# Optimization experiments

Measured on AMD Instinct MI355X. Metric: run time of the kernel, lower is better.

Reference implementation:

```python
import jax, jax.numpy as jnp
import numpy as np

VOCAB, BLOCK, D, H, E, TOPK = 50257, 2048, 1024, 8, 8, 2
HD = D // H  # head_size = 128


def _layernorm(x, g, b, eps=1e-5):
    mu = jnp.mean(x, axis=-1, keepdims=True)
    var = jnp.mean(jnp.square(x - mu), axis=-1, keepdims=True)
    return (x - mu) * jax.lax.rsqrt(var + eps) * g + b


def setup_inputs() -> dict:
    key = jax.random.key(0)
    ks = jax.random.split(key, 12)
    s = 0.02
    return {
        "idx": jax.random.randint(ks[0], (4, BLOCK), 0, VOCAB),
        "tok_table": jax.random.normal(ks[1], (VOCAB, D), jnp.float32) * s,
        "pos_table": jax.random.normal(ks[2], (BLOCK, D), jnp.float32) * s,
        "Wq": jax.random.normal(ks[3], (H, D, HD), jnp.float32) * s,
        "Wk": jax.random.normal(ks[4], (H, D, HD), jnp.float32) * s,
        "Wv": jax.random.normal(ks[5], (H, D, HD), jnp.float32) * s,
        "Wo": jax.random.normal(ks[6], (D, D), jnp.float32) * s,
        "bo": jnp.zeros((D,), jnp.float32),
        "g1": jnp.ones((D,), jnp.float32),
        "b1": jnp.zeros((D,), jnp.float32),
        "g2": jnp.ones((D,), jnp.float32),
        "b2": jnp.zeros((D,), jnp.float32),
        "Wr": jax.random.normal(ks[7], (D, E), jnp.float32) * s,
        "br": jnp.zeros((E,), jnp.float32),
        "Wn": jax.random.normal(ks[8], (D, E), jnp.float32) * s,
        "bn": jnp.zeros((E,), jnp.float32),
    }


def reference(idx, tok_table, pos_table, Wq, Wk, Wv, Wo, bo, g1, b1, g2, b2, Wr, br, Wn, bn):
    B, T = idx.shape
    x = tok_table[idx] + pos_table[:T]  # [B,T,D]

    # --- multi-head causal self-attention (dropout off / eval mode) ---
    xn = _layernorm(x, g1, b1)
    q = jnp.einsum('btc,hcd->bhtd', xn, Wq)
    k = jnp.einsum('btc,hcd->bhtd', xn, Wk)
    v = jnp.einsum('btc,hcd->bhtd', xn, Wv)
    # NOTE: original scales by C**-0.5 where C = n_embed (not head_size)
    wei = jnp.einsum('bhtd,bhsd->bhts', q, k) * (D ** -0.5)
    causal = jnp.tril(jnp.ones((T, T), bool))
    wei = jnp.where(causal, wei, -jnp.inf)
    wei = jax.nn.softmax(wei, axis=-1)
    attn = jnp.einsum('bhts,bhsd->bhtd', wei, v)  # [B,H,T,HD]
    attn = attn.transpose(0, 2, 1, 3).reshape(B, T, D)  # concat heads
    x = x + attn @ Wo + bo  # residual

    x_norm = _layernorm(x, g2, b2)

    # --- noisy top-k router ---
    logits = x_norm @ Wr + br          # [B,T,E]
    noise_logits = x_norm @ Wn + bn    # [B,T,E]
    noise = jax.random.normal(jax.random.key(42), logits.shape, logits.dtype)
    noisy = logits + noise * jax.nn.softplus(noise_logits)
    top_vals, indices = jax.lax.top_k(noisy, TOPK)  # [B,T,K]
    probs_k = jax.nn.softmax(top_vals, axis=-1)     # softmax over -inf-scattered logits == softmax over top-k
    router_probs = jnp.sum(jax.nn.one_hot(indices, E, dtype=probs_k.dtype) * probs_k[..., None], axis=-2)

    return (x_norm, router_probs, indices, x)
```

## Files before the change

### kernel.cpp

```cpp
#include <hip/hip_runtime.h>
#include <math.h>
#include <stdint.h>

typedef __attribute__((ext_vector_type(8))) _Float16 f16x8;
typedef __attribute__((ext_vector_type(4))) _Float16 f16x4;
typedef __attribute__((ext_vector_type(4))) float f32x4;

__device__ __forceinline__ void split_f16(float x, _Float16& h, _Float16& l) {
  h = (_Float16)x;
  l = (_Float16)((x - (float)h) * 2048.0f);
}

__device__ __forceinline__ void gld16(const void* g, void* l) {
  __builtin_amdgcn_global_load_lds(
      (const __attribute__((address_space(1))) void*)g,
      (__attribute__((address_space(3))) void*)l, 16, 0, 0);
}

__device__ __forceinline__ void threefry2x32_42(uint32_t x0, uint32_t x1,
                                                uint32_t& o0, uint32_t& o1) {
  const uint32_t k0 = 0u, k1 = 42u;
  const uint32_t k2 = k0 ^ k1 ^ 0x1BD11BDAu;
  x0 += k0; x1 += k1;
#define TF_R(r) { x0 += x1; x1 = (x1 << (r)) | (x1 >> (32 - (r))); x1 ^= x0; }
  TF_R(13) TF_R(15) TF_R(26) TF_R(6)
  x0 += k1; x1 += k2 + 1u;
  TF_R(17) TF_R(29) TF_R(16) TF_R(24)
  x0 += k2; x1 += k0 + 2u;
  TF_R(13) TF_R(15) TF_R(26) TF_R(6)
  x0 += k0; x1 += k1 + 3u;
  TF_R(17) TF_R(29) TF_R(16) TF_R(24)
  x0 += k1; x1 += k2 + 4u;
  TF_R(13) TF_R(15) TF_R(26) TF_R(6)
  x0 += k2; x1 += k0 + 5u;
#undef TF_R
  o0 = x0; o1 = x1;
}

__device__ __forceinline__ float jax_erfinv_f32(float x) {
  float xx = __fmul_rn(x, x);
  float w = -log1pf(-xx);
  float p;
  if (w < 5.0f) {
    w = __fadd_rn(w, -2.5f);
    p = 2.81022636e-08f;
    p = __fadd_rn(3.43273939e-07f, __fmul_rn(p, w));
    p = __fadd_rn(-3.5233877e-06f, __fmul_rn(p, w));
    p = __fadd_rn(-4.39150654e-06f, __fmul_rn(p, w));
    p = __fadd_rn(0.00021858087f, __fmul_rn(p, w));
    p = __fadd_rn(-0.00125372503f, __fmul_rn(p, w));
    p = __fadd_rn(-0.00417768164f, __fmul_rn(p, w));
    p = __fadd_rn(0.246640727f, __fmul_rn(p, w));
    p = __fadd_rn(1.50140941f, __fmul_rn(p, w));
  } else {
    w = __fadd_rn(sqrtf(w), -3.0f);
    p = -0.000200214257f;
    p = __fadd_rn(0.000100950558f, __fmul_rn(p, w));
    p = __fadd_rn(0.00134934322f, __fmul_rn(p, w));
    p = __fadd_rn(-0.00367342844f, __fmul_rn(p, w));
    p = __fadd_rn(0.00573950773f, __fmul_rn(p, w));
    p = __fadd_rn(-0.0076224613f, __fmul_rn(p, w));
    p = __fadd_rn(0.00943887047f, __fmul_rn(p, w));
    p = __fadd_rn(1.00167406f, __fmul_rn(p, w));
    p = __fadd_rn(2.83297682f, __fmul_rn(p, w));
  }
  return __fmul_rn(p, x);
}

__device__ __forceinline__ float jax_noise(uint32_t n) {
  uint32_t o0, o1;
  threefry2x32_42(0u, n, o0, o1);
  uint32_t bits = o0 ^ o1;
  uint32_t fb = (bits >> 9) | 0x3F800000u;
  float f = __fadd_rn(__uint_as_float(fb), -1.0f);
  const float lo = __uint_as_float(0xBF7FFFFFu);
  float u = __fadd_rn(__fmul_rn(f, 2.0f), lo);
  u = fmaxf(lo, u);
  return __fmul_rn(__uint_as_float(0x3FB504F3u), jax_erfinv_f32(u));
}

__device__ __forceinline__ float block_sum_256(float v, float* buf) {
  #pragma unroll
  for (int off = 32; off > 0; off >>= 1) v += __shfl_down(v, off, 64);
  int lane = threadIdx.x & 63;
  int w = threadIdx.x >> 6;
  if (lane == 0) buf[w] = v;
  __syncthreads();
  return buf[0] + buf[1] + buf[2] + buf[3];
}

__global__ __launch_bounds__(128) void k_wsplit(
    const float* __restrict__ Wq, const float* __restrict__ Wk,
    const float* __restrict__ Wv, const float* __restrict__ Wo,
    _Float16* __restrict__ wqt_h, _Float16* __restrict__ wqt_l,
    _Float16* __restrict__ wot_h, _Float16* __restrict__ wot_l) {
  int z = blockIdx.x, tid = threadIdx.x;
  const float* src;
  int ldn, n;
  _Float16 *dh, *dl;
  if (z < 24) {
    int which = z >> 3, h = z & 7;
    src = ((which == 0) ? Wq : (which == 1) ? Wk : Wv) + (size_t)h * 1024 * 128;
    ldn = 128; n = tid;
    dh = wqt_h + (size_t)z * 128 * 1024 + (size_t)n * 1024;
    dl = wqt_l + (size_t)z * 128 * 1024 + (size_t)n * 1024;
  } else {
    int zz = z - 24;
    src = Wo; ldn = 1024; n = zz * 128 + tid;
    dh = wot_h + (size_t)n * 1024;
    dl = wot_l + (size_t)n * 1024;
  }
  for (int k0 = 0; k0 < 1024; k0 += 16) {
    f16x8 hv0, hv1, lv0, lv1;
    #pragma unroll
    for (int j = 0; j < 8; ++j) {
      _Float16 hh, ll;
      split_f16(src[(size_t)(k0 + j) * ldn + n], hh, ll);
      hv0[j] = hh; lv0[j] = ll;
    }
    #pragma unroll
    for (int j = 0; j < 8; ++j) {
      _Float16 hh, ll;
      split_f16(src[(size_t)(k0 + 8 + j) * ldn + n], hh, ll);
      hv1[j] = hh; lv1[j] = ll;
    }
    *(f16x8*)(dh + k0) = hv0; *(f16x8*)(dh + k0 + 8) = hv1;
    *(f16x8*)(dl + k0) = lv0; *(f16x8*)(dl + k0 + 8) = lv1;
  }
}

__global__ __launch_bounds__(256) void k_embed_ln1(
    const int* __restrict__ idx, const float* __restrict__ tok,
    const float* __restrict__ pos, const float* __restrict__ g1,
    const float* __restrict__ b1, float* __restrict__ x_out,
    _Float16* __restrict__ xnh, _Float16* __restrict__ xnl) {
  __shared__ float bufA[4], bufB[4];
  int r = blockIdx.x;
  int t = r & 2047;
  int token = idx[r];
  int c4 = threadIdx.x;
  float4 tv = *((const float4*)(tok + (size_t)token * 1024) + c4);
  float4 pv = *((const float4*)(pos + (size_t)t * 1024) + c4);
  float4 xv = make_float4(tv.x + pv.x, tv.y + pv.y, tv.z + pv.z, tv.w + pv.w);
  *((float4*)(x_out + (size_t)r * 1024) + c4) = xv;
  float mu = block_sum_256(xv.x + xv.y + xv.z + xv.w, bufA) * (1.0f / 1024.0f);
  float d0 = xv.x - mu, d1 = xv.y - mu, d2 = xv.z - mu, d3 = xv.w - mu;
  float var = block_sum_256(d0*d0 + d1*d1 + d2*d2 + d3*d3, bufB) * (1.0f / 1024.0f);
  float rs = rsqrtf(var + 1e-5f);
  float4 gv = *((const float4*)g1 + c4);
  float4 bv = *((const float4*)b1 + c4);
  float xn0 = d0*rs*gv.x + bv.x, xn1 = d1*rs*gv.y + bv.y;
  float xn2 = d2*rs*gv.z + bv.z, xn3 = d3*rs*gv.w + bv.w;
  f16x4 hv, lv;
  _Float16 hh, ll;
  split_f16(xn0, hh, ll); hv[0] = hh; lv[0] = ll;
  split_f16(xn1, hh, ll); hv[1] = hh; lv[1] = ll;
  split_f16(xn2, hh, ll); hv[2] = hh; lv[2] = ll;
  split_f16(xn3, hh, ll); hv[3] = hh; lv[3] = ll;
  *(f16x4*)(xnh + (size_t)r * 1024 + c4 * 4) = hv;
  *(f16x4*)(xnl + (size_t)r * 1024 + c4 * 4) = lv;
}

__global__ __launch_bounds__(256) void k_ln2(
    const float* __restrict__ x, const float* __restrict__ g2,
    const float* __restrict__ b2, float* __restrict__ xn_out) {
  __shared__ float bufA[4], bufB[4];
  int r = blockIdx.x;
  int c4 = threadIdx.x;
  float4 xv = *((const float4*)(x + (size_t)r * 1024) + c4);
  float mu = block_sum_256(xv.x + xv.y + xv.z + xv.w, bufA) * (1.0f / 1024.0f);
  float d0 = xv.x - mu, d1 = xv.y - mu, d2 = xv.z - mu, d3 = xv.w - mu;
  float var = block_sum_256(d0*d0 + d1*d1 + d2*d2 + d3*d3, bufB) * (1.0f / 1024.0f);
  float rs = rsqrtf(var + 1e-5f);
  float4 gv = *((const float4*)g2 + c4);
  float4 bv = *((const float4*)b2 + c4);
  float4 xn = make_float4(d0*rs*gv.x + bv.x, d1*rs*gv.y + bv.y,
                          d2*rs*gv.z + bv.z, d3*rs*gv.w + bv.w);
  *((float4*)(xn_out + (size_t)r * 1024) + c4) = xn;
}

__global__ __launch_bounds__(256) void k_qkv(
    const _Float16* __restrict__ xnh, const _Float16* __restrict__ xnl,
    const _Float16* __restrict__ wth, const _Float16* __restrict__ wtl,
    _Float16* __restrict__ qh, _Float16* __restrict__ ql,
    _Float16* __restrict__ kh, _Float16* __restrict__ kl,
    _Float16* __restrict__ vth, _Float16* __restrict__ vtl) {
  __shared__ __align__(16) _Float16 Ah[128 * 32], Al[128 * 32];
  __shared__ __align__(16) _Float16 Bh[128 * 32], Bl[128 * 32];
  int z = blockIdx.x;
  int which = z >> 3, h = z & 7;
  int m0 = blockIdx.y * 128;
  int tid = threadIdx.x, w = tid >> 6, lane = tid & 63;
  const _Float16* bsh = wth + (size_t)z * 128 * 1024;
  const _Float16* bsl = wtl + (size_t)z * 128 * 1024;
  f32x4 om[2][8], oc[2][8];
  const f32x4 zero4 = {0.f, 0.f, 0.f, 0.f};
  #pragma unroll
  for (int mr = 0; mr < 2; ++mr)
    #pragma unroll
    for (int nb = 0; nb < 8; ++nb) { om[mr][nb] = zero4; oc[mr][nb] = zero4; }

  for (int k0 = 0; k0 < 1024; k0 += 32) {
    __syncthreads();
    #pragma unroll
    for (int i2 = 0; i2 < 2; ++i2) {
      int r = w * 32 + i2 * 16 + (lane >> 2);
      int gs = (lane & 3) ^ ((r >> 1) & 3);
      size_t ao = (size_t)(m0 + r) * 1024 + k0 + gs * 8;
      size_t bo_ = (size_t)r * 1024 + k0 + gs * 8;
      gld16(xnh + ao, &Ah[(w * 32 + i2 * 16) * 32]);
      gld16(xnl + ao, &Al[(w * 32 + i2 * 16) * 32]);
      gld16(bsh + bo_, &Bh[(w * 32 + i2 * 16) * 32]);
      gld16(bsl + bo_, &Bl[(w * 32 + i2 * 16) * 32]);
    }
    asm volatile("s_waitcnt vmcnt(0)" ::: "memory");
    __syncthreads();
    f16x8 ah[2], al[2];
    #pragma unroll
    for (int mr = 0; mr < 2; ++mr) {
      int arow = w * 32 + mr * 16 + (lane & 15);
      int ag = (lane >> 4) ^ ((arow >> 1) & 3);
      ah[mr] = *(f16x8*)&Ah[arow * 32 + ag * 8];
      al[mr] = *(f16x8*)&Al[arow * 32 + ag * 8];
    }
    #pragma unroll
    for (int nb = 0; nb < 8; ++nb) {
      int brow = nb * 16 + (lane & 15);
      int bg = (lane >> 4) ^ ((brow >> 1) & 3);
      f16x8 b8h = *(f16x8*)&Bh[brow * 32 + bg * 8];
      f16x8 b8l = *(f16x8*)&Bl[brow * 32 + bg * 8];
      #pragma unroll
      for (int mr = 0; mr < 2; ++mr) {
        om[mr][nb] = __builtin_amdgcn_mfma_f32_16x16x32_f16(ah[mr], b8h, om[mr][nb], 0, 0, 0);
        oc[mr][nb] = __builtin_amdgcn_mfma_f32_16x16x32_f16(ah[mr], b8l, oc[mr][nb], 0, 0, 0);
        oc[mr][nb] = __builtin_amdgcn_mfma_f32_16x16x32_f16(al[mr], b8h, oc[mr][nb], 0, 0, 0);
      }
    }
  }
  int bb = m0 >> 11, tb = m0 & 2047;
  if (which < 2) {
    _Float16* OH = (which == 0) ? qh : kh;
    _Float16* OL = (which == 0) ? ql : kl;
    size_t base = (size_t)(bb * 8 + h) * 2048 * 128;
    #pragma unroll
    for (int mr = 0; mr < 2; ++mr)
      #pragma unroll
      for (int r2 = 0; r2 < 4; ++r2) {
        int t = tb + w * 32 + mr * 16 + ((lane >> 4) << 2) + r2;
        size_t roff = base + (size_t)t * 128 + (lane & 15);
        #pragma unroll
        for (int nb = 0; nb < 8; ++nb) {
          float v = om[mr][nb][r2] + oc[mr][nb][r2] * (1.0f / 2048.0f);
          _Float16 hh, ll;
          split_f16(v, hh, ll);
          OH[roff + nb * 16] = hh;
          OL[roff + nb * 16] = ll;
        }
      }
  } else {
    size_t base = (size_t)(bb * 8 + h) * 128 * 2048;
    #pragma unroll
    for (int mr = 0; mr < 2; ++mr) {
      int t4 = tb + w * 32 + mr * 16 + ((lane >> 4) << 2);
      #pragma unroll
      for (int nb = 0; nb < 8; ++nb) {
        int col = nb * 16 + (lane & 15);
        size_t off = base + (size_t)col * 2048 + t4;
        f16x4 hv, lv;
        #pragma unroll
        for (int r2 = 0; r2 < 4; ++r2) {
          _Float16 hh, ll;
          split_f16(om[mr][nb][r2] + oc[mr][nb][r2] * (1.0f / 2048.0f), hh, ll);
          hv[r2] = hh; lv[r2] = ll;
        }
        *(f16x4*)(vth + off) = hv;
        *(f16x4*)(vtl + off) = lv;
      }
    }
  }
}

__global__ __launch_bounds__(256) void k_proj_res(
    const _Float16* __restrict__ ah_, const _Float16* __restrict__ al_,
    const _Float16* __restrict__ wth, const _Float16* __restrict__ wtl,
    const float* __restrict__ bo, float* __restrict__ x_io) {
  __shared__ __align__(16) _Float16 Ah[128 * 64], Al[128 * 64];
  __shared__ __align__(16) _Float16 Bh[128 * 64], Bl[128 * 64];
  int n0 = blockIdx.x * 128;
  int m0 = blockIdx.y * 128;
  int tid = threadIdx.x, w = tid >> 6, lane = tid & 63;
  f32x4 om[2][8], oc[2][8];
  const f32x4 zero4 = {0.f, 0.f, 0.f, 0.f};
  #pragma unroll
  for (int mr = 0; mr < 2; ++mr)
    #pragma unroll
    for (int nb = 0; nb < 8; ++nb) { om[mr][nb] = zero4; oc[mr][nb] = zero4; }

  for (int k0 = 0; k0 < 1024; k0 += 64) {
    __syncthreads();
    #pragma unroll
    for (int i2 = 0; i2 < 4; ++i2) {
      int r = w * 32 + i2 * 8 + (lane >> 3);
      int gs = (lane & 7) ^ (r & 7);
      size_t ao = (size_t)(m0 + r) * 1024 + k0 + gs * 8;
      size_t bo_ = (size_t)(n0 + r) * 1024 + k0 + gs * 8;
      gld16(ah_ + ao, &Ah[(w * 32 + i2 * 8) * 64]);
      gld16(al_ + ao, &Al[(w * 32 + i2 * 8) * 64]);
      gld16(wth + bo_, &Bh[(w * 32 + i2 * 8) * 64]);
      gld16(wtl + bo_, &Bl[(w * 32 + i2 * 8) * 64]);
    }
    asm volatile("s_waitcnt vmcnt(0)" ::: "memory");
    __syncthreads();
    #pragma unroll
    for (int k2 = 0; k2 < 2; ++k2) {
      f16x8 ah[2], al[2];
      #pragma unroll
      for (int mr = 0; mr < 2; ++mr) {
        int arow = w * 32 + mr * 16 + (lane & 15);
        int ag = (k2 * 4 + (lane >> 4)) ^ (arow & 7);
        ah[mr] = *(f16x8*)&Ah[arow * 64 + ag * 8];
        al[mr] = *(f16x8*)&Al[arow * 64 + ag * 8];
      }
      #pragma unroll
      for (int nb = 0; nb < 8; ++nb) {
        int brow = nb * 16 + (lane & 15);
        int bg = (k2 * 4 + (lane >> 4)) ^ (brow & 7);
        f16x8 b8h = *(f16x8*)&Bh[brow * 64 + bg * 8];
        f16x8 b8l = *(f16x8*)&Bl[brow * 64 + bg * 8];
        #pragma unroll
        for (int mr = 0; mr < 2; ++mr) {
          om[mr][nb] = __builtin_amdgcn_mfma_f32_16x16x32_f16(ah[mr], b8h, om[mr][nb], 0, 0, 0);
          oc[mr][nb] = __builtin_amdgcn_mfma_f32_16x16x32_f16(ah[mr], b8l, oc[mr][nb], 0, 0, 0);
          oc[mr][nb] = __builtin_amdgcn_mfma_f32_16x16x32_f16(al[mr], b8h, oc[mr][nb], 0, 0, 0);
        }
      }
    }
  }
  #pragma unroll
  for (int mr = 0; mr < 2; ++mr)
    #pragma unroll
    for (int nb = 0; nb < 8; ++nb) {
      int col = n0 + nb * 16 + (lane & 15);
      float bov = bo[col];
      #pragma unroll
      for (int r2 = 0; r2 < 4; ++r2) {
        int gm = m0 + w * 32 + mr * 16 + ((lane >> 4) << 2) + r2;
        float* p = x_io + (size_t)gm * 1024 + col;
        *p += om[mr][nb][r2] + oc[mr][nb][r2] * (1.0f / 2048.0f) + bov;
      }
    }
}

__global__ __launch_bounds__(256) void k_attn(
    const _Float16* __restrict__ qhp, const _Float16* __restrict__ qlp,
    const _Float16* __restrict__ khp, const _Float16* __restrict__ klp,
    const _Float16* __restrict__ vthp, const _Float16* __restrict__ vtlp,
    _Float16* __restrict__ attn_h, _Float16* __restrict__ attn_l) {
  __shared__ __align__(16) _Float16 Ksh[2][32 * 128];
  __shared__ __align__(16) _Float16 Ksl[2][32 * 128];
  __shared__ __align__(16) _Float16 Vh[2][128 * 32];
  __shared__ __align__(16) _Float16 Vl[2][128 * 32];
  __shared__ __align__(16) _Float16 Ph4[4][16 * 32];
  __shared__ __align__(16) _Float16 Pl4[4][16 * 32];

  int h = blockIdx.y, b = blockIdx.z;
  int qs = blockIdx.x;
  int tid = threadIdx.x;
  int w = tid >> 6, lane = tid & 63;

  size_t bh = (size_t)(b * 8 + h) * 2048 * 128;
  const _Float16* qhb = qhp + bh;
  const _Float16* qlb = qlp + bh;
  const _Float16* khb = khp + bh;
  const _Float16* klb = klp + bh;
  const _Float16* vhb = vthp + bh;
  const _Float16* vlb = vtlp + bh;
  _Float16* Ph = &Ph4[w][0];
  _Float16* Pl = &Pl4[w][0];

  const f32x4 zero4 = {0.f, 0.f, 0.f, 0.f};

  auto stage = [&](int cur, int j0) {
    #pragma unroll
    for (int i2 = 0; i2 < 2; ++i2) {
      int r = w * 8 + i2 * 4 + (lane >> 4);
      int gs = (lane & 15) ^ (r & 7);
      size_t go = (size_t)(j0 + r) * 128 + gs * 8;
      gld16(khb + go, &Ksh[cur][(w * 8 + i2 * 4) * 128]);
      gld16(klb + go, &Ksl[cur][(w * 8 + i2 * 4) * 128]);
    }
    #pragma unroll
    for (int i2 = 0; i2 < 2; ++i2) {
      int r = w * 32 + i2 * 16 + (lane >> 2);
      int gs = (lane & 3) ^ ((r >> 1) & 3);
      size_t go = (size_t)r * 2048 + j0 + gs * 8;
      gld16(vhb + go, &Vh[cur][(w * 32 + i2 * 16) * 32]);
      gld16(vlb + go, &Vl[cur][(w * 32 + i2 * 16) * 32]);
    }
  };

  #pragma unroll 1
  for (int pi = 0; pi < 2; ++pi) {
    int qt = pi ? (31 - qs) : qs;
    int t0 = qt << 6;
    int tW = t0 + w * 16;
    int rowBase = tW + ((lane >> 4) << 2);

    size_t qoff = (size_t)(tW + (lane & 15)) * 128 + ((lane >> 4) << 3);
    f16x8 qfh[4], qfl[4];
    #pragma unroll
    for (int kk = 0; kk < 4; ++kk) {
      qfh[kk] = *(const f16x8*)(qhb + qoff + kk * 32);
      qfl[kk] = *(const f16x8*)(qlb + qoff + kk * 32);
    }

    f32x4 om[8], oc[8];
    #pragma unroll
    for (int db = 0; db < 8; ++db) { om[db] = zero4; oc[db] = zero4; }
    float mreg[4], lreg[4];
    #pragma unroll
    for (int r2 = 0; r2 < 4; ++r2) { mreg[r2] = -INFINITY; lreg[r2] = 0.f; }

    int nt = 2 * qt + 2;
    stage(0, 0);
    asm volatile("s_waitcnt vmcnt(0)" ::: "memory");
    __syncthreads();
    int cur = 0;

    #pragma unroll 1
    for (int t = 0; t < nt; ++t) {
      if (t + 1 < nt) stage(cur ^ 1, (t + 1) * 32);
      int j0 = t * 32;

      f32x4 sm[2], sc[2];
      #pragma unroll
      for (int nb = 0; nb < 2; ++nb) { sm[nb] = zero4; sc[nb] = zero4; }
      #pragma unroll
      for (int kk = 0; kk < 4; ++kk) {
        #pragma unroll
        for (int nb = 0; nb < 2; ++nb) {
          int krow = nb * 16 + (lane & 15);
          int kg = (kk * 4 + (lane >> 4)) ^ (krow & 7);
          f16x8 kfh = *(f16x8*)&Ksh[cur][krow * 128 + kg * 8];
          f16x8 kfl = *(f16x8*)&Ksl[cur][krow * 128 + kg * 8];
          sm[nb] = __builtin_amdgcn_mfma_f32_16x16x32_f16(qfh[kk], kfh, sm[nb], 0, 0, 0);
          sc[nb] = __builtin_amdgcn_mfma_f32_16x16x32_f16(qfh[kk], kfl, sc[nb], 0, 0, 0);
          sc[nb] = __builtin_amdgcn_mfma_f32_16x16x32_f16(qfl[kk], kfh, sc[nb], 0, 0, 0);
        }
      }

      float rmax[4];
      #pragma unroll
      for (int r2 = 0; r2 < 4; ++r2) rmax[r2] = -INFINITY;
      #pragma unroll
      for (int nb = 0; nb < 2; ++nb) {
        int col = j0 + nb * 16 + (lane & 15);
        #pragma unroll
        for (int r2 = 0; r2 < 4; ++r2) {
          float sv = (sm[nb][r2] + sc[nb][r2] * (1.0f / 2048.0f)) * 0.03125f;
          sv = (col > rowBase + r2) ? -INFINITY : sv;
          sm[nb][r2] = sv;
          rmax[r2] = fmaxf(rmax[r2], sv);
        }
      }
      #pragma unroll
      for (int mk = 1; mk < 16; mk <<= 1)
        #pragma unroll
        for (int r2 = 0; r2 < 4; ++r2)
          rmax[r2] = fmaxf(rmax[r2], __shfl_xor(rmax[r2], mk, 64));
      float alpha[4], rsum[4];
      bool newmax = false;
      #pragma unroll
      for (int r2 = 0; r2 < 4; ++r2) {
        float mnew = fmaxf(mreg[r2], rmax[r2]);
        newmax |= (mnew > mreg[r2]);
        alpha[r2] = __expf(mreg[r2] - mnew);
        mreg[r2] = mnew;
        rsum[r2] = 0.f;
      }
      #pragma unroll
      for (int nb = 0; nb < 2; ++nb)
        #pragma unroll
        for (int r2 = 0; r2 < 4; ++r2) {
          float p = __expf(sm[nb][r2] - mreg[r2]);
          sm[nb][r2] = p;
          rsum[r2] += p;
        }
      #pragma unroll
      for (int mk = 1; mk < 16; mk <<= 1)
        #pragma unroll
        for (int r2 = 0; r2 < 4; ++r2)
          rsum[r2] += __shfl_xor(rsum[r2], mk, 64);
      #pragma unroll
      for (int r2 = 0; r2 < 4; ++r2)
        lreg[r2] = lreg[r2] * alpha[r2] + rsum[r2];

      #pragma unroll
      for (int nb = 0; nb < 2; ++nb) {
        int col = nb * 16 + (lane & 15);
        #pragma unroll
        for (int r2 = 0; r2 < 4; ++r2) {
          int prow = ((lane >> 4) << 2) + r2;
          int sg = (col >> 3) ^ ((prow >> 1) & 3);
          float ps = sm[nb][r2] * 16384.0f;
          _Float16 hh, ll;
          split_f16(ps, hh, ll);
          Ph[prow * 32 + sg * 8 + (col & 7)] = hh;
          Pl[prow * 32 + sg * 8 + (col & 7)] = ll;
        }
      }

      if (__any((int)newmax)) {
        #pragma unroll
        for (int db = 0; db < 8; ++db)
          #pragma unroll
          for (int r2 = 0; r2 < 4; ++r2) {
            om[db][r2] *= alpha[r2];
            oc[db][r2] *= alpha[r2];
          }
      }

      {
        int prow = lane & 15;
        int pg = (lane >> 4) ^ ((prow >> 1) & 3);
        f16x8 pah = *(f16x8*)&Ph[prow * 32 + pg * 8];
        f16x8 pal = *(f16x8*)&Pl[prow * 32 + pg * 8];
        #pragma unroll
        for (int db = 0; db < 8; ++db) {
          int vrow = db * 16 + (lane & 15);
          int vg = (lane >> 4) ^ ((vrow >> 1) & 3);
          f16x8 vfh = *(f16x8*)&Vh[cur][vrow * 32 + vg * 8];
          f16x8 vfl = *(f16x8*)&Vl[cur][vrow * 32 + vg * 8];
          om[db] = __builtin_amdgcn_mfma_f32_16x16x32_f16(pah, vfh, om[db], 0, 0, 0);
          oc[db] = __builtin_amdgcn_mfma_f32_16x16x32_f16(pah, vfl, oc[db], 0, 0, 0);
          oc[db] = __builtin_amdgcn_mfma_f32_16x16x32_f16(pal, vfh, oc[db], 0, 0, 0);
        }
      }

      asm volatile("s_waitcnt vmcnt(0)" ::: "memory");
      __syncthreads();
      cur ^= 1;
    }

    size_t obase = ((size_t)(b * 2048 + rowBase)) * 1024 + h * 128 + (lane & 15);
    #pragma unroll
    for (int r2 = 0; r2 < 4; ++r2) {
      float inv = 1.f / (lreg[r2] * 16384.0f);
      #pragma unroll
      for (int db = 0; db < 8; ++db) {
        float v = (om[db][r2] + oc[db][r2] * (1.0f / 2048.0f)) * inv;
        _Float16 hh, ll;
        split_f16(v, hh, ll);
        attn_h[obase + (size_t)r2 * 1024 + db * 16] = hh;
        attn_l[obase + (size_t)r2 * 1024 + db * 16] = ll;
      }
    }
  }
}

__global__ __launch_bounds__(256) void k_router(
    const float* __restrict__ xn, const float* __restrict__ Wr,
    const float* __restrict__ br, const float* __restrict__ Wn,
    const float* __restrict__ bn, float* __restrict__ rp_out,
    float* __restrict__ idx_out) {
  int wave = threadIdx.x >> 6, lane = threadIdx.x & 63;
  int r = blockIdx.x * 4 + wave;
  const float* xr = xn + (size_t)r * 1024;
  float acc[16];
  #pragma unroll
  for (int i = 0; i < 16; ++i) acc[i] = 0.f;
  int cbase = lane * 16;
  for (int cc = 0; cc < 16; ++cc) {
    int c = cbase + cc;
    float xv = xr[c];
    const float4* wr4 = (const float4*)(Wr + (size_t)c * 8);
    float4 w0 = wr4[0], w1 = wr4[1];
    acc[0] += xv * w0.x; acc[1] += xv * w0.y; acc[2] += xv * w0.z; acc[3] += xv * w0.w;
    acc[4] += xv * w1.x; acc[5] += xv * w1.y; acc[6] += xv * w1.z; acc[7] += xv * w1.w;
    const float4* wn4 = (const float4*)(Wn + (size_t)c * 8);
    float4 n0 = wn4[0], n1 = wn4[1];
    acc[8]  += xv * n0.x; acc[9]  += xv * n0.y; acc[10] += xv * n0.z; acc[11] += xv * n0.w;
    acc[12] += xv * n1.x; acc[13] += xv * n1.y; acc[14] += xv * n1.z; acc[15] += xv * n1.w;
  }
  #pragma unroll
  for (int i = 0; i < 16; ++i) {
    #pragma unroll
    for (int off = 32; off > 0; off >>= 1) acc[i] += __shfl_down(acc[i], off, 64);
  }
  if (lane == 0) {
    float noisy[8];
    uint32_t nbase = (uint32_t)r * 8u;
    #pragma unroll
    for (int e = 0; e < 8; ++e) {
      float lg = acc[e] + br[e];
      float x = acc[8 + e] + bn[e];
      float sp = __fadd_rn(fmaxf(x, 0.f), log1pf(expf(-fabsf(x))));
      float nz = jax_noise(nbase + (uint32_t)e);
      noisy[e] = __fadd_rn(lg, __fmul_rn(nz, sp));
    }
    float v1 = -INFINITY, v2 = -INFINITY;
    int i1 = 0, i2 = 0;
    #pragma unroll
    for (int e = 0; e < 8; ++e) {
      float vv = noisy[e];
      if (vv > v1) { v2 = v1; i2 = i1; v1 = vv; i1 = e; }
      else if (vv > v2) { v2 = vv; i2 = e; }
    }
    float e2 = expf(v2 - v1);
    float ssum = 1.f + e2;
    float p1 = 1.f / ssum, p2 = e2 / ssum;
    float rp[8];
    #pragma unroll
    for (int e = 0; e < 8; ++e) rp[e] = 0.f;
    rp[i1] = p1; rp[i2] = p2;
    float* op = rp_out + (size_t)r * 8;
    #pragma unroll
    for (int e = 0; e < 8; ++e) op[e] = rp[e];
    idx_out[(size_t)r * 2]     = (float)i1;
    idx_out[(size_t)r * 2 + 1] = (float)i2;
  }
}

extern "C" void kernel_launch(void* const* d_in, const int* in_sizes, int n_in,
                              void* d_out, int out_size, void* d_ws, size_t ws_size,
                              hipStream_t stream) {
  const int*   idx = (const int*)d_in[0];
  const float* tok = (const float*)d_in[1];
  const float* pos = (const float*)d_in[2];
  const float* Wq  = (const float*)d_in[3];
  const float* Wk  = (const float*)d_in[4];
  const float* Wv  = (const float*)d_in[5];
  const float* Wo  = (const float*)d_in[6];
  const float* bo  = (const float*)d_in[7];
  const float* g1  = (const float*)d_in[8];
  const float* b1  = (const float*)d_in[9];
  const float* g2  = (const float*)d_in[10];
  const float* b2  = (const float*)d_in[11];
  const float* Wr  = (const float*)d_in[12];
  const float* br  = (const float*)d_in[13];
  const float* Wn  = (const float*)d_in[14];
  const float* bn  = (const float*)d_in[15];

  float* out_xnorm = (float*)d_out;
  float* out_rp    = out_xnorm + 8388608;
  float* out_idx   = out_rp + 65536;
  float* out_x     = out_idx + 16384;

  _Float16* xnh  = (_Float16*)d_ws;
  _Float16* xnl  = xnh + 8388608;
  _Float16* qhp  = xnl + 8388608;
  _Float16* qlp  = qhp + 8388608;
  _Float16* khp  = qlp + 8388608;
  _Float16* klp  = khp + 8388608;
  _Float16* vthp = klp + 8388608;
  _Float16* vtlp = vthp + 8388608;
  _Float16* attn_h = xnh;
  _Float16* attn_l = xnl;
  _Float16* wqt_h = (_Float16*)out_xnorm;
  _Float16* wqt_l = wqt_h + 3145728;
  _Float16* wot_h = wqt_l + 3145728;
  _Float16* wot_l = wot_h + 1048576;

  k_wsplit<<<32, 128, 0, stream>>>(Wq, Wk, Wv, Wo, wqt_h, wqt_l, wot_h, wot_l);
  k_embed_ln1<<<8192, 256, 0, stream>>>(idx, tok, pos, g1, b1, out_x, xnh, xnl);
  k_qkv<<<dim3(24, 64), 256, 0, stream>>>(xnh, xnl, wqt_h, wqt_l,
                                          qhp, qlp, khp, klp, vthp, vtlp);
  k_attn<<<dim3(16, 8, 4), 256, 0, stream>>>(qhp, qlp, khp, klp, vthp, vtlp,
                                             attn_h, attn_l);
  k_proj_res<<<dim3(8, 64), 256, 0, stream>>>(attn_h, attn_l, wot_h, wot_l, bo, out_x);
  k_ln2<<<8192, 256, 0, stream>>>(out_x, g2, b2, out_xnorm);
  k_router<<<2048, 256, 0, stream>>>(out_xnorm, Wr, br, Wn, bn, out_rp, out_idx);
}
```

Baseline: 1.085 ms.

## Enlarge attention query tile to 128 rows with 512-thread blocks

```diff
diff --git a/kernel.cpp b/kernel.cpp
--- a/kernel.cpp
+++ b/kernel.cpp
@@ -351,7 +351,7 @@
     }
 }
 
-__global__ __launch_bounds__(256) void k_attn(
+__global__ __launch_bounds__(512) void k_attn(
     const _Float16* __restrict__ qhp, const _Float16* __restrict__ qlp,
     const _Float16* __restrict__ khp, const _Float16* __restrict__ klp,
     const _Float16* __restrict__ vthp, const _Float16* __restrict__ vtlp,
@@ -360,11 +360,12 @@
   __shared__ __align__(16) _Float16 Ksl[2][32 * 128];
   __shared__ __align__(16) _Float16 Vh[2][128 * 32];
   __shared__ __align__(16) _Float16 Vl[2][128 * 32];
-  __shared__ __align__(16) _Float16 Ph4[4][16 * 32];
-  __shared__ __align__(16) _Float16 Pl4[4][16 * 32];
-
-  int h = blockIdx.y, b = blockIdx.z;
-  int qs = blockIdx.x;
+  __shared__ __align__(16) _Float16 Ph8[8][16 * 32];
+  __shared__ __align__(16) _Float16 Pl8[8][16 * 32];
+
+  int bh_ = blockIdx.x;
+  int b = bh_ >> 3, h = bh_ & 7;
+  int qs = blockIdx.y;
   int tid = threadIdx.x;
   int w = tid >> 6, lane = tid & 63;
 
@@ -375,34 +376,28 @@
   const _Float16* klb = klp + bh;
   const _Float16* vhb = vthp + bh;
   const _Float16* vlb = vtlp + bh;
-  _Float16* Ph = &Ph4[w][0];
-  _Float16* Pl = &Pl4[w][0];
+  _Float16* Ph = &Ph8[w][0];
+  _Float16* Pl = &Pl8[w][0];
 
   const f32x4 zero4 = {0.f, 0.f, 0.f, 0.f};
 
   auto stage = [&](int cur, int j0) {
-    #pragma unroll
-    for (int i2 = 0; i2 < 2; ++i2) {
-      int r = w * 8 + i2 * 4 + (lane >> 4);
-      int gs = (lane & 15) ^ (r & 7);
-      size_t go = (size_t)(j0 + r) * 128 + gs * 8;
-      gld16(khb + go, &Ksh[cur][(w * 8 + i2 * 4) * 128]);
-      gld16(klb + go, &Ksl[cur][(w * 8 + i2 * 4) * 128]);
-    }
-    #pragma unroll
-    for (int i2 = 0; i2 < 2; ++i2) {
-      int r = w * 32 + i2 * 16 + (lane >> 2);
-      int gs = (lane & 3) ^ ((r >> 1) & 3);
-      size_t go = (size_t)r * 2048 + j0 + gs * 8;
-      gld16(vhb + go, &Vh[cur][(w * 32 + i2 * 16) * 32]);
-      gld16(vlb + go, &Vl[cur][(w * 32 + i2 * 16) * 32]);
-    }
+    int kr = (w << 2) + (lane >> 4);
+    int kg = (lane & 15) ^ (kr & 7);
+    size_t kgo = (size_t)(j0 + kr) * 128 + kg * 8;
+    gld16(khb + kgo, &Ksh[cur][(w << 2) * 128]);
+    gld16(klb + kgo, &Ksl[cur][(w << 2) * 128]);
+    int vr = (w << 4) + (lane >> 2);
+    int vg = (lane & 3) ^ ((vr >> 1) & 3);
+    size_t vgo = (size_t)vr * 2048 + j0 + vg * 8;
+    gld16(vhb + vgo, &Vh[cur][(w << 4) * 32]);
+    gld16(vlb + vgo, &Vl[cur][(w << 4) * 32]);
   };
 
   #pragma unroll 1
   for (int pi = 0; pi < 2; ++pi) {
-    int qt = pi ? (31 - qs) : qs;
-    int t0 = qt << 6;
+    int qt = pi ? (15 - qs) : qs;
+    int t0 = qt << 7;
     int tW = t0 + w * 16;
     int rowBase = tW + ((lane >> 4) << 2);
 
@@ -421,7 +416,7 @@
     #pragma unroll
     for (int r2 = 0; r2 < 4; ++r2) { mreg[r2] = -INFINITY; lreg[r2] = 0.f; }
 
-    int nt = 2 * qt + 2;
+    int nt = 4 * qt + 4;
     stage(0, 0);
     asm volatile("s_waitcnt vmcnt(0)" ::: "memory");
     __syncthreads();
@@ -665,8 +660,8 @@
   k_embed_ln1<<<8192, 256, 0, stream>>>(idx, tok, pos, g1, b1, out_x, xnh, xnl);
   k_qkv<<<dim3(24, 64), 256, 0, stream>>>(xnh, xnl, wqt_h, wqt_l,
                                           qhp, qlp, khp, klp, vthp, vtlp);
-  k_attn<<<dim3(16, 8, 4), 256, 0, stream>>>(qhp, qlp, khp, klp, vthp, vtlp,
-                                             attn_h, attn_l);
+  k_attn<<<dim3(32, 8), 512, 0, stream>>>(qhp, qlp, khp, klp, vthp, vtlp,
+                                          attn_h, attn_l);
   k_proj_res<<<dim3(8, 64), 256, 0, stream>>>(attn_h, attn_l, wot_h, wot_l, bo, out_x);
   k_ln2<<<8192, 256, 0, stream>>>(out_x, g2, b2, out_xnorm);
   k_router<<<2048, 256, 0, stream>>>(out_xnorm, Wr, br, Wn, bn, out_rp, out_idx);
```

Measured after the change: 967.5 us. 1.12x faster.
